# Performance work log

Measured on AMD Instinct MI355X. Metric: run time of the kernel, lower is better.

## Reference

```python
import jax, jax.numpy as jnp
import numpy as np

NT, NC = 100000, 25000
ETT, ECT = 800000, 400000
DIN_T, DIN_C = 64, 32
H, C = 4, 32
HID = H * C  # 128
SLOPE = 0.2  # GATConv LeakyReLU negative slope


def setup_inputs() -> dict:
    key = jax.random.key(0)
    ks = jax.random.split(key, 24)
    def p(i, shape, s=0.05):
        return jax.random.normal(ks[i], shape, dtype=jnp.float32) * s
    return {
        'x_target': jax.random.normal(ks[0], (NT, DIN_T), dtype=jnp.float32),
        'x_context': jax.random.normal(ks[1], (NC, DIN_C), dtype=jnp.float32),
        'edge_tt': jax.random.randint(ks[2], (2, ETT), 0, NT),
        'edge_ct_src': jax.random.randint(ks[3], (ECT,), 0, NC),
        'edge_ct_dst': jax.random.randint(ks[4], (ECT,), 0, NT),
        'W_pre_t': p(5, (DIN_T, HID)), 'b_pre_t': jnp.zeros((HID,), jnp.float32),
        'W_pre_c': p(6, (DIN_C, HID)), 'b_pre_c': jnp.zeros((HID,), jnp.float32),
        'W_sd': p(7, (HID, HID)), 'att_src_sd': p(8, (H, C)), 'att_dst_sd': p(9, (H, C)), 'b_sd': jnp.zeros((HID,), jnp.float32),
        'W_ds': p(10, (HID, HID)), 'att_src_ds': p(11, (H, C)), 'att_dst_ds': p(12, (H, C)), 'b_ds': jnp.zeros((HID,), jnp.float32),
        'W_ct_src': p(13, (HID, HID)), 'W_ct_dst': p(14, (HID, HID)), 'att_src_ct': p(15, (H, C)), 'att_dst_ct': p(16, (H, C)), 'b_ct': jnp.zeros((HID,), jnp.float32),
        'W_out': p(17, (HID, HID)), 'b_out': jnp.zeros((HID,), jnp.float32),
    }


def _gat(h_src, h_dst, att_s, att_d, src, dst, n_dst, bias):
    # h_src: [N_src,H,C] transformed src feats; h_dst: [N_dst,H,C]
    a_s = jnp.einsum('nhc,hc->nh', h_src, att_s)  # [N_src,H]
    a_d = jnp.einsum('nhc,hc->nh', h_dst, att_d)  # [N_dst,H]
    e = a_s[src] + a_d[dst]                        # [E,H]
    e = jnp.where(e > 0, e, SLOPE * e)             # LeakyReLU(0.2)
    m = jax.ops.segment_max(e, dst, num_segments=n_dst)  # stable softmax per dst
    ex = jnp.exp(e - m[dst])
    den = jax.ops.segment_sum(ex, dst, num_segments=n_dst)
    alpha = ex / den[dst]                          # [E,H]
    msg = h_src[src] * alpha[:, :, None]           # [E,H,C]
    out = jax.ops.segment_sum(msg, dst, num_segments=n_dst)
    return out.reshape(n_dst, H * C) + bias


def reference(x_target, x_context, edge_tt, edge_ct_src, edge_ct_dst,
              W_pre_t, b_pre_t, W_pre_c, b_pre_c,
              W_sd, att_src_sd, att_dst_sd, b_sd,
              W_ds, att_src_ds, att_dst_ds, b_ds,
              W_ct_src, W_ct_dst, att_src_ct, att_dst_ct, b_ct,
              W_out, b_out):
    # HeteroDictLinear pretransform + relu
    h_t = jax.nn.relu(x_target @ W_pre_t + b_pre_t)   # [NT,128]
    h_c = jax.nn.relu(x_context @ W_pre_c + b_pre_c)  # [NC,128]
    res = h_t
    # DirGATConv on (target,to,target): forward + reversed, each w/ self-loops
    loops = jnp.arange(NT)
    src_f = jnp.concatenate([edge_tt[0], loops]); dst_f = jnp.concatenate([edge_tt[1], loops])
    src_r = jnp.concatenate([edge_tt[1], loops]); dst_r = jnp.concatenate([edge_tt[0], loops])
    hs = (h_t @ W_sd).reshape(NT, H, C)
    out_sd = _gat(hs, hs, att_src_sd, att_dst_sd, src_f, dst_f, NT, b_sd)
    hd = (h_t @ W_ds).reshape(NT, H, C)
    out_ds = _gat(hd, hd, att_src_ds, att_dst_ds, src_r, dst_r, NT, b_ds)
    out_tt = 0.5 * out_sd + 0.5 * out_ds  # (1-alpha), alpha with alpha=0.5
    # bipartite GATConv on (context,to,target), no self loops
    hcs = (h_c @ W_ct_src).reshape(NC, H, C)
    htd = (h_t @ W_ct_dst).reshape(NT, H, C)
    out_ct = _gat(hcs, htd, att_src_ct, att_dst_ct, edge_ct_src, edge_ct_dst, NT, b_ct)
    # HeteroConv aggr='mean' over the two edge types hitting 'target'
    x = 0.5 * (out_tt + out_ct)
    x = jax.nn.relu(x + res)  # skip connection + relu
    return x @ W_out + b_out
```

## Files before the change

### kernel.cpp

```cpp
#include <hip/hip_runtime.h>
#include <cstdint>
#include <cstddef>

typedef unsigned short u16;
typedef unsigned int u32;

#define NT 100000
#define NC 25000
#define ETT 800000
#define ECT 400000
#define SLOPE 0.2f
#define LOG2E 1.4426950408889634f
#define OFFS (NT + 4)

#define NBK 782
#define NBLK 256
#define CHT ((ETT + NBLK - 1) / NBLK)
#define CHC ((ECT + NBLK - 1) / NBLK)
#define TOTC (3 * NBK * NBLK)
#define NSB ((TOTC + 4095) / 4096)
#define FILL_CAP 4096

#define GT_BLK ((NT + 31) / 32)
#define GC_BLK ((NC + 31) / 32)

typedef __attribute__((ext_vector_type(8))) short bf16x8;
typedef __attribute__((ext_vector_type(4))) float f32x4;

__device__ __forceinline__ u16 f2bf(float f) {
  u32 u = __float_as_uint(f);
  u32 r = (u >> 16) & 1u;
  return (u16)((u + 0x7fffu + r) >> 16);
}
__device__ __forceinline__ float lof(u32 p) { return __uint_as_float(p << 16); }
__device__ __forceinline__ float hif(u32 p) { return __uint_as_float(p & 0xffff0000u); }

__device__ __forceinline__ void compute_bpre(const int* __restrict__ bsum, int* s_bpre) {
  const int t = threadIdx.x;
  const int v = (t < NSB) ? bsum[t] : 0;
  s_bpre[t] = v;
  __syncthreads();
  for (int d = 1; d < 256; d <<= 1) {
    const int u = (t >= d) ? s_bpre[t - d] : 0;
    __syncthreads();
    s_bpre[t] += u;
    __syncthreads();
  }
  const int incl = s_bpre[t];
  __syncthreads();
  s_bpre[t] = incl - v;
  __syncthreads();
}

__global__ __launch_bounds__(256) void transform_hist_kernel(
    const int* __restrict__ tt_src, const int* __restrict__ tt_dst,
    const int* __restrict__ ect_d, int* __restrict__ cntblk,
    const float* __restrict__ Wsd, const float* __restrict__ AsSd, const float* __restrict__ AdSd,
    const float* __restrict__ Wds, const float* __restrict__ AsDs, const float* __restrict__ AdDs,
    const float* __restrict__ Wout,
    u16* __restrict__ bf_sd, u16* __restrict__ bf_ds, u16* __restrict__ bf_out,
    const float* __restrict__ Wcd, const float* __restrict__ attD,
    const float* __restrict__ bsd, const float* __restrict__ bds, const float* __restrict__ bct,
    float* __restrict__ cbias,
    const float* __restrict__ x_t, const float* __restrict__ Wpt, const float* __restrict__ bpt,
    u16* __restrict__ h_t, float* __restrict__ aD,
    const float* __restrict__ x_c, const float* __restrict__ Wpc, const float* __restrict__ bpc,
    const float* __restrict__ Wcs, const float* __restrict__ attS,
    u16* __restrict__ hc_bf, float* __restrict__ aS_c)
{
  __shared__ float s_a[32][33];
  __shared__ float s_b[32][128];
  __shared__ float s_c[32][132];
  const int t = threadIdx.x;

  if (blockIdx.x < NBLK) {
    int* h = (int*)&s_b[0][0];
    const int b = blockIdx.x;
    for (int i = t; i < 3 * NBK; i += 256) h[i] = 0;
    __syncthreads();
    const int lo = b * CHT, hi = min(lo + CHT, ETT);
    for (int i = lo + t; i < hi; i += 256) {
      atomicAdd(&h[tt_dst[i] >> 7], 1);
      atomicAdd(&h[NBK + (tt_src[i] >> 7)], 1);
    }
    const int lo2 = b * CHC, hi2 = min(lo2 + CHC, ECT);
    for (int i = lo2 + t; i < hi2; i += 256)
      atomicAdd(&h[2 * NBK + (ect_d[i] >> 7)], 1);
    __syncthreads();
    for (int i = t; i < 3 * NBK; i += 256)
      cntblk[(size_t)i * NBLK + b] = h[i];
    return;
  }

  const int b = blockIdx.x - NBLK;

  if (b < 4) {
    if (b == 3) {
      if (t < 128) cbias[t] = 0.25f * bsd[t] + 0.25f * bds[t] + 0.5f * bct[t];
      return;
    }
    float* fS = &s_c[0][0];
    float* fD = fS + 512;
    const float* W = (b == 0) ? Wsd : (b == 1) ? Wds : Wout;
    const float* As = (b == 0) ? AsSd : AsDs;
    const float* Ad = (b == 0) ? AdSd : AdDs;
    u16* out = (b == 0) ? bf_sd : (b == 1) ? bf_ds : bf_out;
    const int tiles = (b == 2) ? 8 : 9;
    if (b < 2) {
      if (t < 128) {
        for (int h = 0; h < 4; ++h) {
          float s1 = 0.f, s2 = 0.f;
          for (int c = 0; c < 32; ++c) {
            const float wv = W[t * 128 + h * 32 + c];
            s1 = fmaf(wv, As[h * 32 + c], s1);
            s2 = fmaf(wv, Ad[h * 32 + c], s2);
          }
          fS[t * 4 + h] = s1 * LOG2E; fD[t * 4 + h] = s2 * LOG2E;
        }
      }
      __syncthreads();
    }
    const int total = tiles * 4 * 64 * 8;
    for (int i = t; i < total; i += 256) {
      const int j = i & 7, lane = (i >> 3) & 63, ks = (i >> 9) & 3, ti = i >> 11;
      const int k = ks * 32 + (lane >> 4) * 8 + j;
      const int n = ti * 16 + (lane & 15);
      float v;
      if (n < 128) v = W[k * 128 + n];
      else if (n < 132) v = fS[k * 4 + (n - 128)];
      else if (n < 136) v = fD[k * 4 + (n - 132)];
      else v = 0.f;
      out[i] = f2bf(v);
    }
    return;
  }

  if (b < 4 + GT_BLK) {
    float* s_fold = &s_c[0][0];
    if (t < 128) {
      for (int h = 0; h < 4; ++h) {
        float s = 0.f;
        for (int c = 0; c < 32; ++c)
          s = fmaf(Wcd[t * 128 + h * 32 + c], attD[h * 32 + c], s);
        s_fold[t * 4 + h] = s * LOG2E;
      }
    }
    const int row0 = (b - 4) * 32;
    const int rl = t >> 3, cg = t & 7;
    const int gr = row0 + rl;
    float acc[4][4];
    for (int g = 0; g < 4; ++g)
      for (int j = 0; j < 4; ++j)
        acc[g][j] = bpt[g * 32 + cg * 4 + j];
    for (int kc = 0; kc < 64; kc += 32) {
      {
        float4 f = make_float4(0.f, 0.f, 0.f, 0.f);
        if (gr < NT) f = *(const float4*)(x_t + (size_t)gr * 64 + kc + cg * 4);
        s_a[rl][cg * 4 + 0] = f.x; s_a[rl][cg * 4 + 1] = f.y;
        s_a[rl][cg * 4 + 2] = f.z; s_a[rl][cg * 4 + 3] = f.w;
      }
      for (int j = 0; j < 4; ++j) {
        const int idx = t + j * 256;
        const int k = idx >> 5, c4 = (idx & 31) * 4;
        *(float4*)&s_b[k][c4] = *(const float4*)(Wpt + (size_t)(kc + k) * 128 + c4);
      }
      __syncthreads();
#pragma unroll 8
      for (int k = 0; k < 32; ++k) {
        const float a = s_a[rl][k];
        for (int g = 0; g < 4; ++g) {
          const float4 w = *(const float4*)&s_b[k][g * 32 + cg * 4];
          acc[g][0] = fmaf(a, w.x, acc[g][0]);
          acc[g][1] = fmaf(a, w.y, acc[g][1]);
          acc[g][2] = fmaf(a, w.z, acc[g][2]);
          acc[g][3] = fmaf(a, w.w, acc[g][3]);
        }
      }
      __syncthreads();
    }
    if (gr < NT) {
      float p0 = 0.f, p1 = 0.f, p2 = 0.f, p3 = 0.f;
      for (int g = 0; g < 4; ++g) {
        for (int j = 0; j < 4; ++j) acc[g][j] = fmaxf(acc[g][j], 0.f);
        uint2 pk;
        pk.x = (u32)f2bf(acc[g][0]) | ((u32)f2bf(acc[g][1]) << 16);
        pk.y = (u32)f2bf(acc[g][2]) | ((u32)f2bf(acc[g][3]) << 16);
        *(uint2*)(h_t + (size_t)gr * 128 + g * 32 + cg * 4) = pk;
        for (int j = 0; j < 4; ++j) {
          const int col = g * 32 + cg * 4 + j;
          const float4 f4 = *(const float4*)&s_fold[col * 4];
          const float a = acc[g][j];
          p0 = fmaf(a, f4.x, p0); p1 = fmaf(a, f4.y, p1);
          p2 = fmaf(a, f4.z, p2); p3 = fmaf(a, f4.w, p3);
        }
      }
      for (int m = 1; m < 8; m <<= 1) {
        p0 += __shfl_xor(p0, m); p1 += __shfl_xor(p1, m);
        p2 += __shfl_xor(p2, m); p3 += __shfl_xor(p3, m);
      }
      if (cg == 0) *(float4*)(aD + (size_t)gr * 4) = make_float4(p0, p1, p2, p3);
    }
    return;
  }

  {
    const int row0 = (b - 4 - GT_BLK) * 32;
    const int rl = t >> 3, cg = t & 7;
    const int gr = row0 + rl;
    {
      float4 f = make_float4(0.f, 0.f, 0.f, 0.f);
      if (gr < NC) f = *(const float4*)(x_c + (size_t)gr * 32 + cg * 4);
      s_a[rl][cg * 4 + 0] = f.x; s_a[rl][cg * 4 + 1] = f.y;
      s_a[rl][cg * 4 + 2] = f.z; s_a[rl][cg * 4 + 3] = f.w;
    }
    for (int j = 0; j < 4; ++j) {
      const int idx = t + j * 256;
      const int k = idx >> 5, c4 = (idx & 31) * 4;
      *(float4*)&s_b[k][c4] = *(const float4*)(Wpc + (size_t)k * 128 + c4);
    }
    __syncthreads();
    float acc[4][4];
    for (int g = 0; g < 4; ++g)
      for (int j = 0; j < 4; ++j) acc[g][j] = bpc[g * 32 + cg * 4 + j];
#pragma unroll 8
    for (int k = 0; k < 32; ++k) {
      const float a = s_a[rl][k];
      for (int g = 0; g < 4; ++g) {
        const float4 w = *(const float4*)&s_b[k][g * 32 + cg * 4];
        acc[g][0] = fmaf(a, w.x, acc[g][0]);
        acc[g][1] = fmaf(a, w.y, acc[g][1]);
        acc[g][2] = fmaf(a, w.z, acc[g][2]);
        acc[g][3] = fmaf(a, w.w, acc[g][3]);
      }
    }
    for (int g = 0; g < 4; ++g)
      *(float4*)&s_c[rl][g * 32 + cg * 4] =
          make_float4(fmaxf(acc[g][0], 0.f), fmaxf(acc[g][1], 0.f),
                      fmaxf(acc[g][2], 0.f), fmaxf(acc[g][3], 0.f));
    __syncthreads();
    float acc2[4][4];
    for (int g = 0; g < 4; ++g)
      for (int j = 0; j < 4; ++j) acc2[g][j] = 0.f;
    for (int kc = 0; kc < 128; kc += 32) {
      for (int j = 0; j < 4; ++j) {
        const int idx = t + j * 256;
        const int k = idx >> 5, c4 = (idx & 31) * 4;
        *(float4*)&s_b[k][c4] = *(const float4*)(Wcs + (size_t)(kc + k) * 128 + c4);
      }
      __syncthreads();
#pragma unroll 8
      for (int k = 0; k < 32; ++k) {
        const float a = s_c[rl][kc + k];
        for (int g = 0; g < 4; ++g) {
          const float4 w = *(const float4*)&s_b[k][g * 32 + cg * 4];
          acc2[g][0] = fmaf(a, w.x, acc2[g][0]);
          acc2[g][1] = fmaf(a, w.y, acc2[g][1]);
          acc2[g][2] = fmaf(a, w.z, acc2[g][2]);
          acc2[g][3] = fmaf(a, w.w, acc2[g][3]);
        }
      }
      __syncthreads();
    }
    if (gr < NC) {
      float pS[4];
      for (int g = 0; g < 4; ++g) {
        uint2 pk;
        pk.x = (u32)f2bf(acc2[g][0]) | ((u32)f2bf(acc2[g][1]) << 16);
        pk.y = (u32)f2bf(acc2[g][2]) | ((u32)f2bf(acc2[g][3]) << 16);
        *(uint2*)(hc_bf + (size_t)gr * 128 + g * 32 + cg * 4) = pk;
        const float4 as4 = *(const float4*)(attS + g * 32 + cg * 4);
        pS[g] = acc2[g][0] * as4.x + acc2[g][1] * as4.y + acc2[g][2] * as4.z + acc2[g][3] * as4.w;
      }
      for (int m = 1; m < 8; m <<= 1)
        for (int g = 0; g < 4; ++g) pS[g] += __shfl_xor(pS[g], m);
      if (cg == 0)
        *(float4*)(aS_c + (size_t)gr * 4) =
            make_float4(pS[0] * LOG2E, pS[1] * LOG2E, pS[2] * LOG2E, pS[3] * LOG2E);
    }
  }
}

__global__ __launch_bounds__(256) void scan2_blk_kernel(const int* __restrict__ in,
    int* __restrict__ out, int* __restrict__ bsum)
{
  const int t = threadIdx.x, b = blockIdx.x;
  const int idx = b * 4096 + t * 16;
  int v[16];
  int s = 0;
  if (idx < TOTC) {
#pragma unroll
    for (int q = 0; q < 4; ++q) {
      const int4 qq = *(const int4*)(in + idx + q * 4);
      v[q * 4 + 0] = s; s += qq.x;
      v[q * 4 + 1] = s; s += qq.y;
      v[q * 4 + 2] = s; s += qq.z;
      v[q * 4 + 3] = s; s += qq.w;
    }
  } else {
    for (int j = 0; j < 16; ++j) v[j] = 0;
  }
  __shared__ int sh[256];
  sh[t] = s;
  __syncthreads();
  for (int d = 1; d < 256; d <<= 1) {
    const int u = (t >= d) ? sh[t - d] : 0;
    __syncthreads();
    sh[t] += u;
    __syncthreads();
  }
  const int excl = (t == 0) ? 0 : sh[t - 1];
  if (idx < TOTC) {
#pragma unroll
    for (int q = 0; q < 4; ++q) {
      int4 qo;
      qo.x = excl + v[q * 4 + 0]; qo.y = excl + v[q * 4 + 1];
      qo.z = excl + v[q * 4 + 2]; qo.w = excl + v[q * 4 + 3];
      *(int4*)(out + idx + q * 4) = qo;
    }
  }
  if (t == 255) bsum[b] = sh[255];
}

__global__ __launch_bounds__(256) void bin_logits2_kernel(
    const int* __restrict__ tt_src, const int* __restrict__ tt_dst,
    const int* __restrict__ ect_s, const int* __restrict__ ect_d,
    const int* __restrict__ scanned, const int* __restrict__ bsum, u32* __restrict__ bin,
    const short* __restrict__ A, const short* __restrict__ Bsd, const short* __restrict__ Bds,
    u16* __restrict__ hs, float* __restrict__ aSsd, float* __restrict__ aDsd,
    u16* __restrict__ hd, float* __restrict__ aSds, float* __restrict__ aDds, int M)
{
  __shared__ __align__(16) float ldsf[4][16][148];
  const int t = threadIdx.x;

  if (blockIdx.x < NBLK) {
    int* cur = (int*)&ldsf[0][0][0];
    int* s_bpre = cur + 3 * NBK;
    compute_bpre(bsum, s_bpre);
    const int b = blockIdx.x;
    for (int i = t; i < 3 * NBK; i += 256) {
      const int idx = i * NBLK + b;
      cur[i] = scanned[idx] + s_bpre[idx >> 12];
    }
    __syncthreads();
    const int lo = b * CHT, hi = min(lo + CHT, ETT);
    for (int i = lo + t; i < hi; i += 256) {
      const int s = tt_src[i], d = tt_dst[i];
      int p = atomicAdd(&cur[d >> 7], 1);
      bin[p] = ((u32)(d & 127) << 17) | (u32)s;
      p = atomicAdd(&cur[NBK + (s >> 7)], 1);
      bin[p] = ((u32)(s & 127) << 17) | (u32)d;
    }
    const int lo2 = b * CHC, hi2 = min(lo2 + CHC, ECT);
    for (int i = lo2 + t; i < hi2; i += 256) {
      const int s = ect_s[i], d = ect_d[i];
      const int p = atomicAdd(&cur[2 * NBK + (d >> 7)], 1);
      bin[p] = ((u32)(d & 127) << 17) | (u32)s;
    }
    return;
  }

  float (*lds)[16][148] = ldsf;
  const int blk = blockIdx.x - NBLK;
  const int wv = t >> 6, lane = t & 63;
  const int quad = lane >> 4, l16 = lane & 15;
  const int row0 = blk * 64 + wv * 16;
  const int arow = min(row0 + l16, M - 1);
  const short* ap = A + (size_t)arow * 128 + quad * 8;
  bf16x8 af[4];
  for (int ks = 0; ks < 4; ++ks) af[ks] = *(const bf16x8*)(ap + ks * 32);
  const int row = row0 + l16;
  const int idx = lane & 7, rr = lane >> 3;
  for (int pass = 0; pass < 2; ++pass) {
    const short* B = pass ? Bds : Bsd;
    u16* outb = pass ? hd : hs;
    float* aS = pass ? aSds : aSsd;
    float* aD = pass ? aDds : aDsd;
    f32x4 acc[9];
    for (int ti = 0; ti < 9; ++ti) acc[ti] = (f32x4){0.f, 0.f, 0.f, 0.f};
    for (int ks = 0; ks < 4; ++ks)
      for (int ti = 0; ti < 9; ++ti) {
        const bf16x8 bf = *(const bf16x8*)(B + ((ti * 4 + ks) * 64 + lane) * 8);
        acc[ti] = __builtin_amdgcn_mfma_f32_16x16x32_bf16(af[ks], bf, acc[ti], 0, 0, 0);
      }
    for (int ti = 0; ti < 9; ++ti)
      for (int r = 0; r < 4; ++r)
        lds[wv][quad * 4 + r][ti * 16 + l16] = acc[ti][r];
    __syncthreads();
    if (row < M) {
      for (int g = 0; g < 8; ++g) {
        const f32x4 v = *(const f32x4*)&lds[wv][l16][g * 16 + quad * 4];
        uint2 pk;
        pk.x = (u32)f2bf(v[0]) | ((u32)f2bf(v[1]) << 16);
        pk.y = (u32)f2bf(v[2]) | ((u32)f2bf(v[3]) << 16);
        *(uint2*)(outb + (size_t)row * 128 + g * 16 + quad * 4) = pk;
      }
    }
    for (int p = 0; p < 2; ++p) {
      const int lr = p * 8 + rr;
      const int n = row0 + lr;
      if (n < M) {
        const float v = lds[wv][lr][128 + idx];
        if (idx < 4) aS[(size_t)n * 4 + idx] = v;
        else aD[(size_t)n * 4 + idx - 4] = v;
      }
    }
    __syncthreads();
  }
}

__global__ __launch_bounds__(256) void bucket_fill_kernel(const int* __restrict__ scanned,
    const int* __restrict__ bsum, const u32* __restrict__ bin,
    int* __restrict__ offs, int* __restrict__ big_el)
{
  __shared__ int s_cnt[128], s_exc[128], s_cur[128], s_bpre[256];
  __shared__ int s_el[FILL_CAP];
  const int t = threadIdx.x;
  compute_bpre(bsum, s_bpre);
  const int rel = blockIdx.x / NBK;
  const int bucket = blockIdx.x - rel * NBK;
  if (t < 128) s_cnt[t] = 0;
  const int bi = blockIdx.x * NBLK;
  const int base = scanned[bi] + s_bpre[bi >> 12];
  const int nxt = (blockIdx.x == 3 * NBK - 1)
                      ? (2 * ETT + ECT)
                      : scanned[bi + NBLK] + s_bpre[(bi + NBLK) >> 12];
  __syncthreads();
  const int size = nxt - base;
  for (int i = t; i < size; i += 256)
    atomicAdd(&s_cnt[bin[base + i] >> 17], 1);
  __syncthreads();
  if (t < 128) s_exc[t] = s_cnt[t];
  __syncthreads();
  for (int d = 1; d < 128; d <<= 1) {
    int v = 0;
    if (t < 128 && t >= d) v = s_exc[t - d];
    __syncthreads();
    if (t < 128) s_exc[t] += v;
    __syncthreads();
  }
  const int relbase = rel * ETT;
  const int obase = base - relbase;
  int* off_rel = offs + (size_t)rel * OFFS;
  const int node0 = bucket * 128;
  if (t < 128) {
    const int excl = s_exc[t] - s_cnt[t];
    s_cur[t] = excl;
    if (node0 + t < NT) off_rel[node0 + t] = obase + excl;
  }
  if (t == 0 && bucket == NBK - 1) off_rel[NT] = obase + size;
  __syncthreads();
  int* el_rel = big_el + relbase;
  if (size <= FILL_CAP) {
    for (int i = t; i < size; i += 256) {
      const u32 e = bin[base + i];
      const int pos = atomicAdd(&s_cur[e >> 17], 1);
      s_el[pos] = (int)(e & 0x1FFFFu);
    }
    __syncthreads();
    for (int i = t; i < size; i += 256)
      el_rel[obase + i] = s_el[i];
  } else {
    for (int i = t; i < size; i += 256) {
      const u32 e = bin[base + i];
      const int pos = atomicAdd(&s_cur[e >> 17], 1);
      el_rel[obase + pos] = (int)(e & 0x1FFFFu);
    }
  }
}

__global__ __launch_bounds__(256) void mfma_out_kernel(
    const short* __restrict__ A, const short* __restrict__ B,
    const float* __restrict__ bias, float* __restrict__ out, int M)
{
  __shared__ __align__(16) float lds[4][16][132];
  const int wv = threadIdx.x >> 6, lane = threadIdx.x & 63;
  const int quad = lane >> 4, l16 = lane & 15;
  const int row0 = blockIdx.x * 64 + wv * 16;
  const int arow = min(row0 + l16, M - 1);
  const short* ap = A + (size_t)arow * 128 + quad * 8;
  bf16x8 af[4];
  for (int ks = 0; ks < 4; ++ks) af[ks] = *(const bf16x8*)(ap + ks * 32);
  f32x4 acc[8];
  for (int t = 0; t < 8; ++t) acc[t] = (f32x4){0.f, 0.f, 0.f, 0.f};
  for (int ks = 0; ks < 4; ++ks)
    for (int t = 0; t < 8; ++t) {
      const bf16x8 bf = *(const bf16x8*)(B + ((t * 4 + ks) * 64 + lane) * 8);
      acc[t] = __builtin_amdgcn_mfma_f32_16x16x32_bf16(af[ks], bf, acc[t], 0, 0, 0);
    }
  for (int t = 0; t < 8; ++t)
    for (int r = 0; r < 4; ++r)
      lds[wv][quad * 4 + r][t * 16 + l16] = acc[t][r];
  __syncthreads();
  const int row = row0 + l16;
  if (row < M) {
    for (int g = 0; g < 8; ++g) {
      const int col = g * 16 + quad * 4;
      f32x4 v = *(const f32x4*)&lds[wv][l16][col];
      const f32x4 b4 = *(const f32x4*)(bias + col);
      v = v + b4;
      *(f32x4*)(out + (size_t)row * 128 + col) = v;
    }
  }
}

__device__ __forceinline__ void gat_pipe16(const int* __restrict__ off,
    const int* __restrict__ el, const float* __restrict__ aS, const float* __restrict__ aD,
    const u16* __restrict__ hb, int d, int h, int cb, int self_loop, float w,
    float* __restrict__ acc)
{
  const float ad = aD[(size_t)d * 4 + h];
  const int beg = off[d];
  const int m = off[d + 1] - beg;
  const int cnt = m + self_loop;
  if (cnt <= 0) return;
  float den = 0.f;
  float a0 = 0.f, a1 = 0.f, a2 = 0.f, a3 = 0.f, a4 = 0.f, a5 = 0.f, a6 = 0.f, a7 = 0.f;
  int sB = (1 < m) ? el[beg + 1] : d;
  {
    const int sA0 = (0 < m) ? el[beg] : d;
    float eA = aS[(size_t)sA0 * 4 + h];
    uint4 pA = *(const uint4*)(hb + (size_t)sA0 * 128 + cb);
    for (int k = 0; k < cnt; ++k) {
      const int sC = (k + 2 < m) ? el[beg + k + 2] : d;
      const float eB = aS[(size_t)sB * 4 + h];
      const uint4 pB = *(const uint4*)(hb + (size_t)sB * 128 + cb);
      float ea = eA + ad;
      ea = ea > 0.f ? ea : SLOPE * ea;
      const float ex = exp2f(ea);
      den += ex;
      a0 = fmaf(ex, lof(pA.x), a0); a1 = fmaf(ex, hif(pA.x), a1);
      a2 = fmaf(ex, lof(pA.y), a2); a3 = fmaf(ex, hif(pA.y), a3);
      a4 = fmaf(ex, lof(pA.z), a4); a5 = fmaf(ex, hif(pA.z), a5);
      a6 = fmaf(ex, lof(pA.w), a6); a7 = fmaf(ex, hif(pA.w), a7);
      eA = eB; pA = pB; sB = sC;
    }
  }
  const float s = w / den;
  acc[0] = fmaf(a0, s, acc[0]); acc[1] = fmaf(a1, s, acc[1]);
  acc[2] = fmaf(a2, s, acc[2]); acc[3] = fmaf(a3, s, acc[3]);
  acc[4] = fmaf(a4, s, acc[4]); acc[5] = fmaf(a5, s, acc[5]);
  acc[6] = fmaf(a6, s, acc[6]); acc[7] = fmaf(a7, s, acc[7]);
}

__global__ __launch_bounds__(256) void gather_all_kernel(
    const int* __restrict__ off_f, const int* __restrict__ el_f,
    const float* __restrict__ aS_sd, const float* __restrict__ aD_sd, const u16* __restrict__ hs,
    const int* __restrict__ off_r, const int* __restrict__ el_r,
    const float* __restrict__ aS_ds, const float* __restrict__ aD_ds, const u16* __restrict__ hd,
    const int* __restrict__ off_c, const int* __restrict__ el_c,
    const float* __restrict__ aS_ct, const float* __restrict__ aD_ct, const u16* __restrict__ hc,
    const u16* __restrict__ skip, const float* __restrict__ cbias, u16* __restrict__ x)
{
  const int d = blockIdx.x * 16 + (threadIdx.x >> 4);
  if (d >= NT) return;
  const int lg = threadIdx.x & 15;
  const int h = lg >> 2;
  const int cb = lg * 8;
  float acc[8];
  for (int i = 0; i < 8; ++i) acc[i] = 0.f;
  gat_pipe16(off_f, el_f, aS_sd, aD_sd, hs, d, h, cb, 1, 0.25f, acc);
  gat_pipe16(off_r, el_r, aS_ds, aD_ds, hd, d, h, cb, 1, 0.25f, acc);
  gat_pipe16(off_c, el_c, aS_ct, aD_ct, hc, d, h, cb, 0, 0.5f, acc);
  const uint4 sk = *(const uint4*)(skip + (size_t)d * 128 + cb);
  const float4 cb0 = *(const float4*)(cbias + cb);
  const float4 cb1 = *(const float4*)(cbias + cb + 4);
  const float o0 = fmaxf(acc[0] + cb0.x + lof(sk.x), 0.f);
  const float o1 = fmaxf(acc[1] + cb0.y + hif(sk.x), 0.f);
  const float o2 = fmaxf(acc[2] + cb0.z + lof(sk.y), 0.f);
  const float o3 = fmaxf(acc[3] + cb0.w + hif(sk.y), 0.f);
  const float o4 = fmaxf(acc[4] + cb1.x + lof(sk.z), 0.f);
  const float o5 = fmaxf(acc[5] + cb1.y + hif(sk.z), 0.f);
  const float o6 = fmaxf(acc[6] + cb1.z + lof(sk.w), 0.f);
  const float o7 = fmaxf(acc[7] + cb1.w + hif(sk.w), 0.f);
  uint4 r;
  r.x = (u32)f2bf(o0) | ((u32)f2bf(o1) << 16);
  r.y = (u32)f2bf(o2) | ((u32)f2bf(o3) << 16);
  r.z = (u32)f2bf(o4) | ((u32)f2bf(o5) << 16);
  r.w = (u32)f2bf(o6) | ((u32)f2bf(o7) << 16);
  *(uint4*)(x + (size_t)d * 128 + cb) = r;
}

extern "C" void kernel_launch(void* const* d_in, const int* in_sizes, int n_in,
                              void* d_out, int out_size, void* d_ws, size_t ws_size,
                              hipStream_t stream)
{
  const float* x_t   = (const float*)d_in[0];
  const float* x_c   = (const float*)d_in[1];
  const int*   e_tt  = (const int*)d_in[2];
  const int*   ect_s = (const int*)d_in[3];
  const int*   ect_d = (const int*)d_in[4];
  const float* Wpt = (const float*)d_in[5];   const float* bpt = (const float*)d_in[6];
  const float* Wpc = (const float*)d_in[7];   const float* bpc = (const float*)d_in[8];
  const float* Wsd = (const float*)d_in[9];   const float* As_sd = (const float*)d_in[10];
  const float* Ad_sd = (const float*)d_in[11]; const float* bsd = (const float*)d_in[12];
  const float* Wds = (const float*)d_in[13];  const float* As_ds = (const float*)d_in[14];
  const float* Ad_ds = (const float*)d_in[15]; const float* bds = (const float*)d_in[16];
  const float* Wcs = (const float*)d_in[17];  const float* Wcd = (const float*)d_in[18];
  const float* As_ct = (const float*)d_in[19]; const float* Ad_ct = (const float*)d_in[20];
  const float* bct = (const float*)d_in[21];
  const float* Wout = (const float*)d_in[22]; const float* bout = (const float*)d_in[23];

  char* p = (char*)d_ws;
  size_t off = 0;
  auto alloc = [&](size_t bytes) { char* r = p + off; off += (bytes + 255) & ~(size_t)255; return r; };
  u16* ht_bf   = (u16*)alloc((size_t)NT * 128 * 2);
  u16* hs_bf   = (u16*)alloc((size_t)NT * 128 * 2);
  u16* hd_bf   = (u16*)alloc((size_t)NT * 128 * 2);
  u16* hc_bf   = (u16*)alloc((size_t)NC * 128 * 2);
  u16* x_bf    = (u16*)alloc((size_t)NT * 128 * 2);
  float* aS_sd = (float*)alloc((size_t)NT * 4 * 4);
  float* aD_sd = (float*)alloc((size_t)NT * 4 * 4);
  float* aS_ds = (float*)alloc((size_t)NT * 4 * 4);
  float* aD_ds = (float*)alloc((size_t)NT * 4 * 4);
  float* aS_ct = (float*)alloc((size_t)NC * 4 * 4);
  float* aD_ct = (float*)alloc((size_t)NT * 4 * 4);
  int* cntblk  = (int*)alloc((size_t)TOTC * 4);
  int* scanned = (int*)alloc((size_t)TOTC * 4);
  u32* bin     = (u32*)alloc((size_t)(2 * ETT + ECT) * 4);
  int* big_el  = (int*)alloc((size_t)(2 * ETT + ECT) * 4);
  int* offs    = (int*)alloc((size_t)3 * OFFS * 4);
  int* bsum    = (int*)alloc((size_t)NSB * 4);
  float* cbias   = (float*)alloc(128 * 4);
  u16* bfrag_sd  = (u16*)alloc((size_t)9 * 4 * 64 * 8 * 2);
  u16* bfrag_ds  = (u16*)alloc((size_t)9 * 4 * 64 * 8 * 2);
  u16* bfrag_out = (u16*)alloc((size_t)8 * 4 * 64 * 8 * 2);

  int* off_f = offs;
  int* off_r = offs + OFFS;
  int* off_c = offs + 2 * OFFS;
  int* el_f = big_el;
  int* el_r = big_el + ETT;
  int* el_c = big_el + 2 * ETT;

  const int* tt_src = e_tt;
  const int* tt_dst = e_tt + ETT;

  const int gM = (NT + 63) / 64;

  transform_hist_kernel<<<NBLK + 4 + GT_BLK + GC_BLK, 256, 0, stream>>>(
      tt_src, tt_dst, ect_d, cntblk,
      Wsd, As_sd, Ad_sd, Wds, As_ds, Ad_ds, Wout,
      bfrag_sd, bfrag_ds, bfrag_out,
      Wcd, Ad_ct, bsd, bds, bct, cbias,
      x_t, Wpt, bpt, ht_bf, aD_ct,
      x_c, Wpc, bpc, Wcs, As_ct, hc_bf, aS_ct);

  scan2_blk_kernel<<<NSB, 256, 0, stream>>>(cntblk, scanned, bsum);

  bin_logits2_kernel<<<NBLK + gM, 256, 0, stream>>>(
      tt_src, tt_dst, ect_s, ect_d, scanned, bsum, bin,
      (const short*)ht_bf, (const short*)bfrag_sd, (const short*)bfrag_ds,
      hs_bf, aS_sd, aD_sd, hd_bf, aS_ds, aD_ds, NT);

  bucket_fill_kernel<<<3 * NBK, 256, 0, stream>>>(scanned, bsum, bin, offs, big_el);

  gather_all_kernel<<<(NT + 15) / 16, 256, 0, stream>>>(
      off_f, el_f, aS_sd, aD_sd, hs_bf,
      off_r, el_r, aS_ds, aD_ds, hd_bf,
      off_c, el_c, aS_ct, aD_ct, hc_bf,
      ht_bf, cbias, x_bf);

  mfma_out_kernel<<<gM, 256, 0, stream>>>((const short*)x_bf, (const short*)bfrag_out,
                                          bout, (float*)d_out, NT);
}
```

Baseline: 411.7 us.

## Register-block pre-transform GEMMs to 4x8 outputs per thread over 64-row tiles

The dense pre-transform paths (target and context projections) now process 64 rows per block instead of 32. Each thread computes a 4-row by 8-column register tile, reading transposed activations from shared memory as float4s, so every shared-memory load feeds more FMAs. The shared buffers are merged into one byte array with manual carving, and the context block loads its first weight tile before the barrier. This cuts shared-memory traffic per FMA and halves the block count, at the cost of more registers and a 51 KB static shared allocation that may limit occupancy for the histogram blocks in the same kernel.

```diff
diff --git a/kernel.cpp b/kernel.cpp
--- a/kernel.cpp
+++ b/kernel.cpp
@@ -21,8 +21,8 @@
 #define NSB ((TOTC + 4095) / 4096)
 #define FILL_CAP 4096
 
-#define GT_BLK ((NT + 31) / 32)
-#define GC_BLK ((NC + 31) / 32)
+#define PT_BLK ((NT + 63) / 64)
+#define CT_BLK ((NC + 63) / 64)
 
 typedef __attribute__((ext_vector_type(8))) short bf16x8;
 typedef __attribute__((ext_vector_type(4))) float f32x4;
@@ -68,13 +68,11 @@
     const float* __restrict__ Wcs, const float* __restrict__ attS,
     u16* __restrict__ hc_bf, float* __restrict__ aS_c)
 {
-  __shared__ float s_a[32][33];
-  __shared__ float s_b[32][128];
-  __shared__ float s_c[32][132];
+  __shared__ __align__(16) char smem[51200];
   const int t = threadIdx.x;
 
   if (blockIdx.x < NBLK) {
-    int* h = (int*)&s_b[0][0];
+    int* h = (int*)smem;
     const int b = blockIdx.x;
     for (int i = t; i < 3 * NBK; i += 256) h[i] = 0;
     __syncthreads();
@@ -99,7 +97,7 @@
       if (t < 128) cbias[t] = 0.25f * bsd[t] + 0.25f * bds[t] + 0.5f * bct[t];
       return;
     }
-    float* fS = &s_c[0][0];
+    float* fS = (float*)smem;
     float* fD = fS + 512;
     const float* W = (b == 0) ? Wsd : (b == 1) ? Wds : Wout;
     const float* As = (b == 0) ? AsSd : AsDs;
@@ -108,14 +106,14 @@
     const int tiles = (b == 2) ? 8 : 9;
     if (b < 2) {
       if (t < 128) {
-        for (int h = 0; h < 4; ++h) {
+        for (int hh = 0; hh < 4; ++hh) {
           float s1 = 0.f, s2 = 0.f;
           for (int c = 0; c < 32; ++c) {
-            const float wv = W[t * 128 + h * 32 + c];
-            s1 = fmaf(wv, As[h * 32 + c], s1);
-            s2 = fmaf(wv, Ad[h * 32 + c], s2);
+            const float wv = W[t * 128 + hh * 32 + c];
+            s1 = fmaf(wv, As[hh * 32 + c], s1);
+            s2 = fmaf(wv, Ad[hh * 32 + c], s2);
           }
-          fS[t * 4 + h] = s1 * LOG2E; fD[t * 4 + h] = s2 * LOG2E;
+          fS[t * 4 + hh] = s1 * LOG2E; fD[t * 4 + hh] = s2 * LOG2E;
         }
       }
       __syncthreads();
@@ -135,147 +133,206 @@
     return;
   }
 
-  if (b < 4 + GT_BLK) {
-    float* s_fold = &s_c[0][0];
+  if (b < 4 + PT_BLK) {
+    float (*s_xt)[68] = (float(*)[68])smem;
+    float (*s_W)[128] = (float(*)[128])(smem + 17408);
+    float* s_fold     = (float*)(smem + 17408 + 16384);
+    const int row0 = (b - 4) * 64;
+    for (int g = 0; g < 4; ++g) {
+      const int lr = g * 16 + (t >> 4);
+      const int k4 = (t & 15) * 4;
+      const int grow = row0 + lr;
+      float4 f = make_float4(0.f, 0.f, 0.f, 0.f);
+      if (grow < NT) f = *(const float4*)(x_t + (size_t)grow * 64 + k4);
+      s_xt[k4 + 0][lr] = f.x; s_xt[k4 + 1][lr] = f.y;
+      s_xt[k4 + 2][lr] = f.z; s_xt[k4 + 3][lr] = f.w;
+    }
     if (t < 128) {
-      for (int h = 0; h < 4; ++h) {
+      for (int hh = 0; hh < 4; ++hh) {
         float s = 0.f;
         for (int c = 0; c < 32; ++c)
-          s = fmaf(Wcd[t * 128 + h * 32 + c], attD[h * 32 + c], s);
-        s_fold[t * 4 + h] = s * LOG2E;
-      }
-    }
-    const int row0 = (b - 4) * 32;
-    const int rl = t >> 3, cg = t & 7;
-    const int gr = row0 + rl;
-    float acc[4][4];
-    for (int g = 0; g < 4; ++g)
-      for (int j = 0; j < 4; ++j)
-        acc[g][j] = bpt[g * 32 + cg * 4 + j];
+          s = fmaf(Wcd[t * 128 + hh * 32 + c], attD[hh * 32 + c], s);
+        s_fold[t * 4 + hh] = s * LOG2E;
+      }
+    }
+    const int rg = t >> 4;
+    const int cg = t & 15;
+    float acc[4][8];
+    for (int r = 0; r < 4; ++r)
+      for (int j = 0; j < 8; ++j)
+        acc[r][j] = bpt[cg * 4 + (j & 3) + (j >> 2) * 64];
     for (int kc = 0; kc < 64; kc += 32) {
-      {
-        float4 f = make_float4(0.f, 0.f, 0.f, 0.f);
-        if (gr < NT) f = *(const float4*)(x_t + (size_t)gr * 64 + kc + cg * 4);
-        s_a[rl][cg * 4 + 0] = f.x; s_a[rl][cg * 4 + 1] = f.y;
-        s_a[rl][cg * 4 + 2] = f.z; s_a[rl][cg * 4 + 3] = f.w;
-      }
       for (int j = 0; j < 4; ++j) {
         const int idx = t + j * 256;
         const int k = idx >> 5, c4 = (idx & 31) * 4;
-        *(float4*)&s_b[k][c4] = *(const float4*)(Wpt + (size_t)(kc + k) * 128 + c4);
+        *(float4*)&s_W[k][c4] = *(const float4*)(Wpt + (size_t)(kc + k) * 128 + c4);
       }
       __syncthreads();
 #pragma unroll 8
       for (int k = 0; k < 32; ++k) {
-        const float a = s_a[rl][k];
-        for (int g = 0; g < 4; ++g) {
-          const float4 w = *(const float4*)&s_b[k][g * 32 + cg * 4];
-          acc[g][0] = fmaf(a, w.x, acc[g][0]);
-          acc[g][1] = fmaf(a, w.y, acc[g][1]);
-          acc[g][2] = fmaf(a, w.z, acc[g][2]);
-          acc[g][3] = fmaf(a, w.w, acc[g][3]);
+        const float4 xa = *(const float4*)&s_xt[kc + k][rg * 4];
+        const float4 w0 = *(const float4*)&s_W[k][cg * 4];
+        const float4 w1 = *(const float4*)&s_W[k][cg * 4 + 64];
+        const float xr[4] = {xa.x, xa.y, xa.z, xa.w};
+        for (int r = 0; r < 4; ++r) {
+          acc[r][0] = fmaf(xr[r], w0.x, acc[r][0]);
+          acc[r][1] = fmaf(xr[r], w0.y, acc[r][1]);
+          acc[r][2] = fmaf(xr[r], w0.z, acc[r][2]);
+          acc[r][3] = fmaf(xr[r], w0.w, acc[r][3]);
+          acc[r][4] = fmaf(xr[r], w1.x, acc[r][4]);
+          acc[r][5] = fmaf(xr[r], w1.y, acc[r][5]);
+          acc[r][6] = fmaf(xr[r], w1.z, acc[r][6]);
+          acc[r][7] = fmaf(xr[r], w1.w, acc[r][7]);
         }
       }
       __syncthreads();
     }
-    if (gr < NT) {
+    float4 fc0[2], fc1[2];
+    fc0[0] = *(const float4*)&s_fold[(cg * 4 + 0) * 4];
+    (void)fc0; (void)fc1;
+    for (int r = 0; r < 4; ++r) {
+      const int grow = row0 + rg * 4 + r;
+      float v[8];
+      for (int j = 0; j < 8; ++j) v[j] = fmaxf(acc[r][j], 0.f);
       float p0 = 0.f, p1 = 0.f, p2 = 0.f, p3 = 0.f;
-      for (int g = 0; g < 4; ++g) {
-        for (int j = 0; j < 4; ++j) acc[g][j] = fmaxf(acc[g][j], 0.f);
+      for (int j = 0; j < 8; ++j) {
+        const int col = cg * 4 + (j & 3) + ((j >> 2) * 64);
+        const float4 f4 = *(const float4*)&s_fold[col * 4];
+        p0 = fmaf(v[j], f4.x, p0); p1 = fmaf(v[j], f4.y, p1);
+        p2 = fmaf(v[j], f4.z, p2); p3 = fmaf(v[j], f4.w, p3);
+      }
+      if (grow < NT) {
         uint2 pk;
-        pk.x = (u32)f2bf(acc[g][0]) | ((u32)f2bf(acc[g][1]) << 16);
-        pk.y = (u32)f2bf(acc[g][2]) | ((u32)f2bf(acc[g][3]) << 16);
-        *(uint2*)(h_t + (size_t)gr * 128 + g * 32 + cg * 4) = pk;
-        for (int j = 0; j < 4; ++j) {
-          const int col = g * 32 + cg * 4 + j;
-          const float4 f4 = *(const float4*)&s_fold[col * 4];
-          const float a = acc[g][j];
-          p0 = fmaf(a, f4.x, p0); p1 = fmaf(a, f4.y, p1);
-          p2 = fmaf(a, f4.z, p2); p3 = fmaf(a, f4.w, p3);
-        }
-      }
-      for (int m = 1; m < 8; m <<= 1) {
+        pk.x = (u32)f2bf(v[0]) | ((u32)f2bf(v[1]) << 16);
+        pk.y = (u32)f2bf(v[2]) | ((u32)f2bf(v[3]) << 16);
+        *(uint2*)(h_t + (size_t)grow * 128 + cg * 4) = pk;
+        pk.x = (u32)f2bf(v[4]) | ((u32)f2bf(v[5]) << 16);
+        pk.y = (u32)f2bf(v[6]) | ((u32)f2bf(v[7]) << 16);
+        *(uint2*)(h_t + (size_t)grow * 128 + cg * 4 + 64) = pk;
+      }
+      for (int m = 1; m < 16; m <<= 1) {
         p0 += __shfl_xor(p0, m); p1 += __shfl_xor(p1, m);
         p2 += __shfl_xor(p2, m); p3 += __shfl_xor(p3, m);
       }
-      if (cg == 0) *(float4*)(aD + (size_t)gr * 4) = make_float4(p0, p1, p2, p3);
+      if (cg == 0 && grow < NT)
+        *(float4*)(aD + (size_t)grow * 4) = make_float4(p0, p1, p2, p3);
     }
     return;
   }
 
   {
-    const int row0 = (b - 4 - GT_BLK) * 32;
-    const int rl = t >> 3, cg = t & 7;
-    const int gr = row0 + rl;
-    {
+    float (*s_ht)[68]  = (float(*)[68])smem;
+    float (*s_W2)[128] = (float(*)[128])(smem + 34816);
+    float (*s_xc)[68]  = (float(*)[68])smem;
+    const int row0 = (b - 4 - PT_BLK) * 64;
+    for (int g = 0; g < 2; ++g) {
+      const int lr = g * 32 + (t >> 3);
+      const int k4 = (t & 7) * 4;
+      const int grow = row0 + lr;
       float4 f = make_float4(0.f, 0.f, 0.f, 0.f);
-      if (gr < NC) f = *(const float4*)(x_c + (size_t)gr * 32 + cg * 4);
-      s_a[rl][cg * 4 + 0] = f.x; s_a[rl][cg * 4 + 1] = f.y;
-      s_a[rl][cg * 4 + 2] = f.z; s_a[rl][cg * 4 + 3] = f.w;
+      if (grow < NC) f = *(const float4*)(x_c + (size_t)grow * 32 + k4);
+      s_xc[k4 + 0][lr] = f.x; s_xc[k4 + 1][lr] = f.y;
+      s_xc[k4 + 2][lr] = f.z; s_xc[k4 + 3][lr] = f.w;
     }
     for (int j = 0; j < 4; ++j) {
       const int idx = t + j * 256;
       const int k = idx >> 5, c4 = (idx & 31) * 4;
-      *(float4*)&s_b[k][c4] = *(const float4*)(Wpc + (size_t)k * 128 + c4);
-    }
-    __syncthreads();
-    float acc[4][4];
-    for (int g = 0; g < 4; ++g)
-      for (int j = 0; j < 4; ++j) acc[g][j] = bpc[g * 32 + cg * 4 + j];
+      *(float4*)&s_W2[k][c4] = *(const float4*)(Wpc + (size_t)k * 128 + c4);
+    }
+    __syncthreads();
+    const int rg = t >> 4, cg = t & 15;
+    float acc1[4][8];
+    for (int r = 0; r < 4; ++r)
+      for (int j = 0; j < 8; ++j)
+        acc1[r][j] = bpc[cg * 4 + (j & 3) + (j >> 2) * 64];
 #pragma unroll 8
     for (int k = 0; k < 32; ++k) {
-      const float a = s_a[rl][k];
-      for (int g = 0; g < 4; ++g) {
-        const float4 w = *(const float4*)&s_b[k][g * 32 + cg * 4];
-        acc[g][0] = fmaf(a, w.x, acc[g][0]);
-        acc[g][1] = fmaf(a, w.y, acc[g][1]);
-        acc[g][2] = fmaf(a, w.z, acc[g][2]);
-        acc[g][3] = fmaf(a, w.w, acc[g][3]);
-      }
-    }
-    for (int g = 0; g < 4; ++g)
-      *(float4*)&s_c[rl][g * 32 + cg * 4] =
-          make_float4(fmaxf(acc[g][0], 0.f), fmaxf(acc[g][1], 0.f),
-                      fmaxf(acc[g][2], 0.f), fmaxf(acc[g][3], 0.f));
-    __syncthreads();
-    float acc2[4][4];
-    for (int g = 0; g < 4; ++g)
-      for (int j = 0; j < 4; ++j) acc2[g][j] = 0.f;
+      const float4 xa = *(const float4*)&s_xc[k][rg * 4];
+      const float4 w0 = *(const float4*)&s_W2[k][cg * 4];
+      const float4 w1 = *(const float4*)&s_W2[k][cg * 4 + 64];
+      const float xr[4] = {xa.x, xa.y, xa.z, xa.w};
+      for (int r = 0; r < 4; ++r) {
+        acc1[r][0] = fmaf(xr[r], w0.x, acc1[r][0]);
+        acc1[r][1] = fmaf(xr[r], w0.y, acc1[r][1]);
+        acc1[r][2] = fmaf(xr[r], w0.z, acc1[r][2]);
+        acc1[r][3] = fmaf(xr[r], w0.w, acc1[r][3]);
+        acc1[r][4] = fmaf(xr[r], w1.x, acc1[r][4]);
+        acc1[r][5] = fmaf(xr[r], w1.y, acc1[r][5]);
+        acc1[r][6] = fmaf(xr[r], w1.z, acc1[r][6]);
+        acc1[r][7] = fmaf(xr[r], w1.w, acc1[r][7]);
+      }
+    }
+    __syncthreads();
+    for (int r = 0; r < 4; ++r) {
+      const int lr = rg * 4 + r;
+      for (int j = 0; j < 8; ++j) {
+        const int col = cg * 4 + (j & 3) + ((j >> 2) * 64);
+        s_ht[col][lr] = fmaxf(acc1[r][j], 0.f);
+      }
+    }
+    for (int j = 0; j < 4; ++j) {
+      const int idx = t + j * 256;
+      const int k = idx >> 5, c4 = (idx & 31) * 4;
+      *(float4*)&s_W2[k][c4] = *(const float4*)(Wcs + (size_t)k * 128 + c4);
+    }
+    __syncthreads();
+    float acc2[4][8];
+    for (int r = 0; r < 4; ++r)
+      for (int j = 0; j < 8; ++j) acc2[r][j] = 0.f;
     for (int kc = 0; kc < 128; kc += 32) {
-      for (int j = 0; j < 4; ++j) {
-        const int idx = t + j * 256;
-        const int k = idx >> 5, c4 = (idx & 31) * 4;
-        *(float4*)&s_b[k][c4] = *(const float4*)(Wcs + (size_t)(kc + k) * 128 + c4);
-      }
-      __syncthreads();
 #pragma unroll 8
       for (int k = 0; k < 32; ++k) {
-        const float a = s_c[rl][kc + k];
-        for (int g = 0; g < 4; ++g) {
-          const float4 w = *(const float4*)&s_b[k][g * 32 + cg * 4];
-          acc2[g][0] = fmaf(a, w.x, acc2[g][0]);
-          acc2[g][1] = fmaf(a, w.y, acc2[g][1]);
-          acc2[g][2] = fmaf(a, w.z, acc2[g][2]);
-          acc2[g][3] = fmaf(a, w.w, acc2[g][3]);
+        const float4 xa = *(const float4*)&s_ht[kc + k][rg * 4];
+        const float4 w0 = *(const float4*)&s_W2[k][cg * 4];
+        const float4 w1 = *(const float4*)&s_W2[k][cg * 4 + 64];
+        const float xr[4] = {xa.x, xa.y, xa.z, xa.w};
+        for (int r = 0; r < 4; ++r) {
+          acc2[r][0] = fmaf(xr[r], w0.x, acc2[r][0]);
+          acc2[r][1] = fmaf(xr[r], w0.y, acc2[r][1]);
+          acc2[r][2] = fmaf(xr[r], w0.z, acc2[r][2]);
+          acc2[r][3] = fmaf(xr[r], w0.w, acc2[r][3]);
+          acc2[r][4] = fmaf(xr[r], w1.x, acc2[r][4]);
+          acc2[r][5] = fmaf(xr[r], w1.y, acc2[r][5]);
+          acc2[r][6] = fmaf(xr[r], w1.z, acc2[r][6]);
+          acc2[r][7] = fmaf(xr[r], w1.w, acc2[r][7]);
         }
       }
-      __syncthreads();
-    }
-    if (gr < NC) {
-      float pS[4];
-      for (int g = 0; g < 4; ++g) {
+      if (kc < 96) {
+        __syncthreads();
+        for (int j = 0; j < 4; ++j) {
+          const int idx = t + j * 256;
+          const int k = idx >> 5, c4 = (idx & 31) * 4;
+          *(float4*)&s_W2[k][c4] = *(const float4*)(Wcs + (size_t)(kc + 32 + k) * 128 + c4);
+        }
+        __syncthreads();
+      }
+    }
+    const int h2 = cg >> 3;
+    const float4 at0 = *(const float4*)(attS + cg * 4);
+    const float4 at1 = *(const float4*)(attS + cg * 4 + 64);
+    for (int r = 0; r < 4; ++r) {
+      const int grow = row0 + rg * 4 + r;
+      float pa = acc2[r][0] * at0.x + acc2[r][1] * at0.y +
+                 acc2[r][2] * at0.z + acc2[r][3] * at0.w;
+      float pb = acc2[r][4] * at1.x + acc2[r][5] * at1.y +
+                 acc2[r][6] * at1.z + acc2[r][7] * at1.w;
+      if (grow < NC) {
         uint2 pk;
-        pk.x = (u32)f2bf(acc2[g][0]) | ((u32)f2bf(acc2[g][1]) << 16);
-        pk.y = (u32)f2bf(acc2[g][2]) | ((u32)f2bf(acc2[g][3]) << 16);
-        *(uint2*)(hc_bf + (size_t)gr * 128 + g * 32 + cg * 4) = pk;
-        const float4 as4 = *(const float4*)(attS + g * 32 + cg * 4);
-        pS[g] = acc2[g][0] * as4.x + acc2[g][1] * as4.y + acc2[g][2] * as4.z + acc2[g][3] * as4.w;
-      }
-      for (int m = 1; m < 8; m <<= 1)
-        for (int g = 0; g < 4; ++g) pS[g] += __shfl_xor(pS[g], m);
-      if (cg == 0)
-        *(float4*)(aS_c + (size_t)gr * 4) =
-            make_float4(pS[0] * LOG2E, pS[1] * LOG2E, pS[2] * LOG2E, pS[3] * LOG2E);
+        pk.x = (u32)f2bf(acc2[r][0]) | ((u32)f2bf(acc2[r][1]) << 16);
+        pk.y = (u32)f2bf(acc2[r][2]) | ((u32)f2bf(acc2[r][3]) << 16);
+        *(uint2*)(hc_bf + (size_t)grow * 128 + cg * 4) = pk;
+        pk.x = (u32)f2bf(acc2[r][4]) | ((u32)f2bf(acc2[r][5]) << 16);
+        pk.y = (u32)f2bf(acc2[r][6]) | ((u32)f2bf(acc2[r][7]) << 16);
+        *(uint2*)(hc_bf + (size_t)grow * 128 + cg * 4 + 64) = pk;
+      }
+      for (int m = 1; m < 8; m <<= 1) {
+        pa += __shfl_xor(pa, m);
+        pb += __shfl_xor(pb, m);
+      }
+      if ((cg & 7) == 0 && grow < NC) {
+        aS_c[(size_t)grow * 4 + h2] = pa * LOG2E;
+        aS_c[(size_t)grow * 4 + 2 + h2] = pb * LOG2E;
+      }
     }
   }
 }
@@ -637,7 +694,7 @@
 
   const int gM = (NT + 63) / 64;
 
-  transform_hist_kernel<<<NBLK + 4 + GT_BLK + GC_BLK, 256, 0, stream>>>(
+  transform_hist_kernel<<<NBLK + 4 + PT_BLK + CT_BLK, 256, 0, stream>>>(
       tt_src, tt_dst, ect_d, cntblk,
       Wsd, As_sd, Ad_sd, Wds, As_ds, Ad_ds, Wout,
       bfrag_sd, bfrag_ds, bfrag_out,
```

Result: faster. 375.7 us (-8.8%).
